# Kernel tuning notes

Measured on AMD Instinct MI355X. Metric: run time of the kernel, lower is better.

## Reference

```python
import jax, jax.numpy as jnp
import numpy as np

# ---- static config (matches init_kwargs) ----
B, H, W = 4, 256, 256
TIN, F, P = 10, 4, 8          # time steps in, forecast steps, patch size
CIN = TIN + 2                  # x concatenated with 2-channel grid
E = 768                        # LATENT_DIMS
NB, BS = 8, 96                 # num_blocks, block_size = E // NB
HP, WP = H // P, W // P
MID = 4 * E                    # channel-mixer hidden (MLP_RATIO=4)
DEPTH = 4
LAM = 0.01                     # softshrink sparsity_threshold


def _gelu(t):
    return jax.nn.gelu(t, approximate=False)  # torch default GELU (erf)


def _shrink(t):
    return jnp.sign(t) * jnp.maximum(jnp.abs(t) - LAM, 0.0)


def _spectral(x, w1, b1, w2, b2):
    """SpectralConvBlockDiag: rfft2 -> block-diag complex MLP (GELU) -> softshrink -> irfft2 + residual."""
    bias = x
    b_, h_, w_, c_ = x.shape
    wf = w_ // 2 + 1
    xf = jnp.fft.rfft2(x, axes=(1, 2), norm='ortho').reshape(b_, h_, wf, NB, BS)
    xr, xi = jnp.real(xf), jnp.imag(xf)
    mm = lambda t, w: jnp.einsum('bhfni,nio->bhfno', t, w)
    # complex linear 1 + GELU on real/imag separately
    o1r = _gelu(mm(xr, w1[0]) - mm(xi, w1[1]) + b1[0])
    o1i = _gelu(mm(xi, w1[0]) + mm(xr, w1[1]) + b1[1])
    # complex linear 2 + softshrink
    o2r = _shrink(mm(o1r, w2[0]) - mm(o1i, w2[1]) + b2[0])
    o2i = _shrink(mm(o1i, w2[0]) + mm(o1r, w2[1]) + b2[1])
    xf = (o2r + 1j * o2i).reshape(b_, h_, wf, c_)
    out = jnp.fft.irfft2(xf, s=(h_, w_), axes=(1, 2), norm='ortho')
    return out + bias


def setup_inputs() -> dict:
    key = jax.random.key(0)
    ks = jax.random.split(key, 20)
    s = 0.02
    f32 = jnp.float32
    return {
        'x': jax.random.normal(ks[0], (B, H, W, TIN), f32),
        'grid': jax.random.uniform(ks[1], (B, H, W, 2), f32),
        'conv_w': s * jax.random.normal(ks[2], (E, CIN, P, P), f32),
        'conv_b': s * jax.random.normal(ks[3], (E,), f32),
        'pos_emb': s * jax.random.normal(ks[4], (HP, WP, E), f32),
        'w1': s * jax.random.normal(ks[5], (DEPTH, 2, NB, BS, BS), f32),
        'b1': s * jax.random.normal(ks[6], (DEPTH, 2, NB, BS), f32),
        'w2': s * jax.random.normal(ks[7], (DEPTH, 2, NB, BS, BS), f32),
        'b2': s * jax.random.normal(ks[8], (DEPTH, 2, NB, BS), f32),
        'fc1_w': s * jax.random.normal(ks[9], (DEPTH, E, MID), f32),
        'fc1_b': s * jax.random.normal(ks[10], (DEPTH, MID), f32),
        'fc2_w': s * jax.random.normal(ks[11], (DEPTH, MID, E), f32),
        'fc2_b': s * jax.random.normal(ks[12], (DEPTH, E), f32),
        'head_w1': s * jax.random.normal(ks[13], (E, 2 * E), f32),
        'head_b1': s * jax.random.normal(ks[14], (2 * E,), f32),
        'head_w2': s * jax.random.normal(ks[15], (2 * E, P * P), f32),
        'head_b2': s * jax.random.normal(ks[16], (P * P,), f32),
    }


def reference(x, grid, conv_w, conv_b, pos_emb, w1, b1, w2, b2,
              fc1_w, fc1_b, fc2_w, fc2_b, head_w1, head_b1, head_w2, head_b2):
    # concat grid channels and patch-embed (conv stride==kernel == patch einsum)
    z = jnp.concatenate([x, grid], axis=-1)                  # (B,H,W,CIN)
    patches = z.reshape(B, HP, P, WP, P, CIN)
    t = jnp.einsum('bhpwqc,ecpq->bhwe', patches, conv_w) + conv_b + pos_emb  # (B,HP,WP,E)
    states = []
    for _ in range(F):
        for d in range(DEPTH):                               # AFNOBoundariesBlock (no residual, identity norms)
            t = _spectral(t, w1[d], b1[d], w2[d], b2[d])
            t = _gelu(t @ fc1_w[d] + fc1_b[d]) @ fc2_w[d] + fc2_b[d]
        states.append(t)
    ls = jnp.stack(states, axis=1)                           # (B,F,HP,WP,E)
    h = _gelu(ls @ head_w1 + head_b1) @ head_w2 + head_b2    # (B,F,HP,WP,P*P)
    h = h.reshape(B, F, HP, WP, P, P, 1)
    h = jnp.transpose(h, (0, 6, 2, 4, 3, 5, 1)).reshape(B, 1, H, W, F)
    return jnp.squeeze(h, axis=1)                            # (B,H,W,F)
```

## Files before the change

### kernel.cpp

```cpp
#include <hip/hip_runtime.h>
#include <hip/hip_bf16.h>
#include <math.h>


typedef __attribute__((ext_vector_type(8))) _Float16 half8;
typedef __attribute__((ext_vector_type(4))) _Float16 half4v;
typedef __attribute__((ext_vector_type(4))) float float4v;

__device__ __forceinline__ float gelu_f(float v) {
    return 0.5f * v * (1.0f + erff(v * 0.70710678118654752f));
}
__device__ __forceinline__ float shrink_f(float v) {
    return (v > 0.01f) ? (v - 0.01f) : ((v < -0.01f) ? (v + 0.01f) : 0.0f);
}

#define STEP32 0.19634954084936207f

__device__ __forceinline__ void async16(const void* g, void* l) {
    __builtin_amdgcn_global_load_lds(
        (const __attribute__((address_space(1))) unsigned int*)g,
        (__attribute__((address_space(3))) unsigned int*)l, 16, 0, 0);
}

__global__ __launch_bounds__(256) void gather_patch(const float* __restrict__ x,
        const float* __restrict__ grd, _Float16* __restrict__ A)
{
    int idx = blockIdx.x * 256 + threadIdx.x;
    int j   = idx % 768;
    int tok = idx / 768;
    int c = j >> 6, p = (j >> 3) & 7, q = j & 7;
    int wp = tok & 31, hp = (tok >> 5) & 31, b = tok >> 10;
    int hh = hp * 8 + p, ww = wp * 8 + q;
    float v;
    if (c < 10) v = x[((b * 256 + hh) * 256 + ww) * 10 + c];
    else        v = grd[((b * 256 + hh) * 256 + ww) * 2 + (c - 10)];
    A[idx] = (_Float16)v;
}

__global__ __launch_bounds__(256) void dft_fwd_w(const _Float16* __restrict__ th,
        _Float16* __restrict__ Xr, _Float16* __restrict__ Xi)
{
    __shared__ float2 lut[32];
    int bh = blockIdx.x;
    int tid = threadIdx.x;
    if (tid < 32) { float a = tid * STEP32; lut[tid] = make_float2(cosf(a), sinf(a)); }
    __syncthreads();
    int b = bh >> 5, h = bh & 31;
    int c = blockIdx.y * 256 + tid;
    float v[32];
    #pragma unroll
    for (int w = 0; w < 32; ++w) v[w] = (float)th[(bh * 32 + w) * 768 + c];
    for (int kw = 0; kw <= 16; ++kw) {
        float ar = 0.f, ai = 0.f;
        #pragma unroll
        for (int w = 0; w < 32; ++w) {
            float2 cs = lut[(kw * w) & 31];
            ar += v[w] * cs.x;
            ai -= v[w] * cs.y;
        }
        size_t g = ((size_t)(b * 17 + kw) * 32 + h) * 768 + c;
        Xr[g] = (_Float16)(ar * 0.03125f);
        Xi[g] = (_Float16)(ai * 0.03125f);
    }
}

__global__ __launch_bounds__(256) void idft_w_mfma(const _Float16* __restrict__ Yr,
        const _Float16* __restrict__ Yi, _Float16* __restrict__ th)
{
    __shared__ alignas(16) _Float16 Yt[192 * 40];
    __shared__ alignas(16) _Float16 El[32 * 40];

    const int tid  = threadIdx.x;
    const int wave = tid >> 6;
    const int lane = tid & 63;
    const int lr   = lane & 15;
    const int quad = lane >> 4;

    const int bh = blockIdx.x;
    const int b  = bh >> 5, h = bh & 31;
    const int c0 = blockIdx.y * 192;

    for (int i = tid; i < 1024; i += 256) {
        int w = i >> 5, s = i & 31;
        float val;
        if (s <= 16) {
            float g = (s == 0 || s == 16) ? 1.f : 2.f;
            val = g * cosf(((w * s) & 31) * STEP32) * 0.03125f;
        } else {
            int k = s - 16;
            val = -2.f * sinf(((w * k) & 31) * STEP32) * 0.03125f;
        }
        El[w * 40 + s] = (_Float16)val;
    }

    #pragma unroll
    for (int i = 0; i < 3; ++i) {
        int u    = tid + i * 256;
        int slot = u / 24;
        int cg   = u % 24;
        const _Float16* src;
        if (slot < 17) src = Yr + ((size_t)(b * 17 + slot) * 32 + h) * 768;
        else           src = Yi + ((size_t)(b * 17 + (slot - 16)) * 32 + h) * 768;
        half8 v = *(const half8*)(src + c0 + cg * 8);
        #pragma unroll
        for (int e = 0; e < 8; ++e) {
            int el = e ^ (cg & 7);
            Yt[(cg * 8 + el) * 40 + slot] = v[el];
        }
    }
    __syncthreads();

    half8 af[2], bf[3];
    #pragma unroll
    for (int m = 0; m < 2; ++m)
        af[m] = *(const half8*)&El[(m * 16 + lr) * 40 + quad * 8];
    #pragma unroll
    for (int n = 0; n < 3; ++n)
        bf[n] = *(const half8*)&Yt[(wave * 48 + n * 16 + lr) * 40 + quad * 8];
    float4v acc[2][3];
    #pragma unroll
    for (int m = 0; m < 2; ++m)
        #pragma unroll
        for (int n = 0; n < 3; ++n) {
            float4v z = {0.f, 0.f, 0.f, 0.f};
            acc[m][n] = __builtin_amdgcn_mfma_f32_16x16x32_f16(af[m], bf[n], z, 0, 0, 0);
        }

    #pragma unroll
    for (int m = 0; m < 2; ++m)
        #pragma unroll
        for (int n = 0; n < 3; ++n) {
            int c = c0 + wave * 48 + n * 16 + lr;
            #pragma unroll
            for (int r = 0; r < 4; ++r) {
                int w = m * 16 + quad * 4 + r;
                size_t gi = (size_t)(bh * 32 + w) * 768 + c;
                th[gi] = (_Float16)(acc[m][n][r] + (float)th[gi]);
            }
        }
}

__global__ __launch_bounds__(256) void prep_specw(const float* __restrict__ w1,
        const float* __restrict__ w2, _Float16* __restrict__ out)
{
    __shared__ float tile[96][97];
    int mid = blockIdx.x;
    int n  = mid & 7;
    int ri = (mid >> 3) & 1;
    int l  = (mid >> 4) & 1;
    int d  = mid >> 5;
    const float* src = (l ? w2 : w1) + ((size_t)(d * 2 + ri) * 8 + n) * 9216;
    for (int idx = threadIdx.x; idx < 9216; idx += 256)
        tile[idx / 96][idx % 96] = src[idx];
    __syncthreads();
    _Float16* dst = out + (size_t)mid * 9216;
    for (int idx = threadIdx.x; idx < 9216; idx += 256)
        dst[idx] = (_Float16)tile[idx % 96][idx / 96];
}

__global__ __launch_bounds__(256) void spec_fused(
        _Float16* __restrict__ Xr, _Float16* __restrict__ Xi,
        const _Float16* __restrict__ W1r, const _Float16* __restrict__ W1i,
        const _Float16* __restrict__ W2r, const _Float16* __restrict__ W2i,
        const float* __restrict__ b1r, const float* __restrict__ b1i,
        const float* __restrict__ b2r, const float* __restrict__ b2i)
{
    __shared__ alignas(16) _Float16 Ec[1024], Es[1024];
    __shared__ alignas(16) _Float16 XTr[3840], XTi[3840];
    __shared__ alignas(16) _Float16 Zr[3328], Zi[3328];
    __shared__ alignas(16) _Float16 Sr[3328], Si[3328];

    const int bk = blockIdx.x;
    const int n  = blockIdx.y;
    const int tid = threadIdx.x;
    const int wave = tid >> 6, lane = tid & 63;
    const int wr = wave >> 1, wc = wave & 1;
    const int lr = lane & 15, quad = lane >> 4;
    const size_t base = (size_t)bk * 24576 + n * 96;

    for (int i = tid; i < 1024; i += 256) {
        int kh = i >> 5, h = i & 31;
        float a = ((kh * h) & 31) * STEP32;
        Ec[i] = (_Float16)cosf(a);
        Es[i] = (_Float16)sinf(a);
    }
    for (int i = tid; i < 384; i += 256) {
        int h = i / 12, cc = (i % 12) * 8;
        half8 vr = *(const half8*)(Xr + base + (size_t)h * 768 + cc);
        half8 vi = *(const half8*)(Xi + base + (size_t)h * 768 + cc);
        #pragma unroll
        for (int e = 0; e < 8; ++e) {
            XTr[(cc + e) * 40 + h] = vr[e];
            XTi[(cc + e) * 40 + h] = vi[e];
        }
    }
    __syncthreads();

    const _Float16* w1r = W1r + (size_t)n * 9216;
    const _Float16* w1i = W1i + (size_t)n * 9216;
    const _Float16* w2r = W2r + (size_t)n * 9216;
    const _Float16* w2i = W2i + (size_t)n * 9216;

    half8 eC = *(const half8*)&Ec[(wr * 16 + lr) * 32 + quad * 8];
    half8 eS = *(const half8*)&Es[(wr * 16 + lr) * 32 + quad * 8];
    half8 eSn = -eS;

    {
        float4v zr[3], zi[3];
        #pragma unroll
        for (int j = 0; j < 3; ++j) { float4v z = {0,0,0,0}; zr[j] = z; zi[j] = z; }
        #pragma unroll
        for (int j = 0; j < 3; ++j) {
            int c = wc * 48 + j * 16 + lr;
            half8 xr = *(const half8*)&XTr[c * 40 + quad * 8];
            half8 xi = *(const half8*)&XTi[c * 40 + quad * 8];
            zr[j] = __builtin_amdgcn_mfma_f32_16x16x32_f16(eC,  xr, zr[j], 0, 0, 0);
            zr[j] = __builtin_amdgcn_mfma_f32_16x16x32_f16(eS,  xi, zr[j], 0, 0, 0);
            zi[j] = __builtin_amdgcn_mfma_f32_16x16x32_f16(eC,  xi, zi[j], 0, 0, 0);
            zi[j] = __builtin_amdgcn_mfma_f32_16x16x32_f16(eSn, xr, zi[j], 0, 0, 0);
        }
        #pragma unroll
        for (int j = 0; j < 3; ++j) {
            int c = wc * 48 + j * 16 + lr;
            #pragma unroll
            for (int r = 0; r < 4; ++r) {
                int kh = wr * 16 + quad * 4 + r;
                Zr[kh * 104 + c] = (_Float16)zr[j][r];
                Zi[kh * 104 + c] = (_Float16)zi[j][r];
            }
        }
    }
    __syncthreads();

    {
        float4v sr[3], si[3];
        #pragma unroll
        for (int j = 0; j < 3; ++j) { float4v z = {0,0,0,0}; sr[j] = z; si[j] = z; }
        #pragma unroll
        for (int kc = 0; kc < 3; ++kc) {
            half8 ar = *(const half8*)&Zr[(wr * 16 + lr) * 104 + kc * 32 + quad * 8];
            half8 ai = *(const half8*)&Zi[(wr * 16 + lr) * 104 + kc * 32 + quad * 8];
            half8 ain = -ai;
            #pragma unroll
            for (int j = 0; j < 3; ++j) {
                int o = wc * 48 + j * 16 + lr;
                half8 br = *(const half8*)&w1r[o * 96 + kc * 32 + quad * 8];
                half8 bi = *(const half8*)&w1i[o * 96 + kc * 32 + quad * 8];
                sr[j] = __builtin_amdgcn_mfma_f32_16x16x32_f16(ar,  br, sr[j], 0, 0, 0);
                sr[j] = __builtin_amdgcn_mfma_f32_16x16x32_f16(ain, bi, sr[j], 0, 0, 0);
                si[j] = __builtin_amdgcn_mfma_f32_16x16x32_f16(ai,  br, si[j], 0, 0, 0);
                si[j] = __builtin_amdgcn_mfma_f32_16x16x32_f16(ar,  bi, si[j], 0, 0, 0);
            }
        }
        #pragma unroll
        for (int j = 0; j < 3; ++j) {
            int o = wc * 48 + j * 16 + lr;
            float br = b1r[n * 96 + o], bi = b1i[n * 96 + o];
            #pragma unroll
            for (int r = 0; r < 4; ++r) {
                int kh = wr * 16 + quad * 4 + r;
                Sr[kh * 104 + o] = (_Float16)gelu_f(sr[j][r] + br);
                Si[kh * 104 + o] = (_Float16)gelu_f(si[j][r] + bi);
            }
        }
    }
    __syncthreads();

    {
        float4v tr[3], ti[3];
        #pragma unroll
        for (int j = 0; j < 3; ++j) { float4v z = {0,0,0,0}; tr[j] = z; ti[j] = z; }
        #pragma unroll
        for (int kc = 0; kc < 3; ++kc) {
            half8 ar = *(const half8*)&Sr[(wr * 16 + lr) * 104 + kc * 32 + quad * 8];
            half8 ai = *(const half8*)&Si[(wr * 16 + lr) * 104 + kc * 32 + quad * 8];
            half8 ain = -ai;
            #pragma unroll
            for (int j = 0; j < 3; ++j) {
                int o = wc * 48 + j * 16 + lr;
                half8 br = *(const half8*)&w2r[o * 96 + kc * 32 + quad * 8];
                half8 bi = *(const half8*)&w2i[o * 96 + kc * 32 + quad * 8];
                tr[j] = __builtin_amdgcn_mfma_f32_16x16x32_f16(ar,  br, tr[j], 0, 0, 0);
                tr[j] = __builtin_amdgcn_mfma_f32_16x16x32_f16(ain, bi, tr[j], 0, 0, 0);
                ti[j] = __builtin_amdgcn_mfma_f32_16x16x32_f16(ai,  br, ti[j], 0, 0, 0);
                ti[j] = __builtin_amdgcn_mfma_f32_16x16x32_f16(ar,  bi, ti[j], 0, 0, 0);
            }
        }
        #pragma unroll
        for (int j = 0; j < 3; ++j) {
            int o = wc * 48 + j * 16 + lr;
            float br = b2r[n * 96 + o], bi = b2i[n * 96 + o];
            #pragma unroll
            for (int r = 0; r < 4; ++r) {
                int kh = wr * 16 + quad * 4 + r;
                XTr[o * 40 + kh] = (_Float16)shrink_f(tr[j][r] + br);
                XTi[o * 40 + kh] = (_Float16)shrink_f(ti[j][r] + bi);
            }
        }
    }
    __syncthreads();

    {
        float4v yr[3], yi[3];
        #pragma unroll
        for (int j = 0; j < 3; ++j) { float4v z = {0,0,0,0}; yr[j] = z; yi[j] = z; }
        #pragma unroll
        for (int j = 0; j < 3; ++j) {
            int c = wc * 48 + j * 16 + lr;
            half8 t2r = *(const half8*)&XTr[c * 40 + quad * 8];
            half8 t2i = *(const half8*)&XTi[c * 40 + quad * 8];
            yr[j] = __builtin_amdgcn_mfma_f32_16x16x32_f16(eC,  t2r, yr[j], 0, 0, 0);
            yr[j] = __builtin_amdgcn_mfma_f32_16x16x32_f16(eSn, t2i, yr[j], 0, 0, 0);
            yi[j] = __builtin_amdgcn_mfma_f32_16x16x32_f16(eC,  t2i, yi[j], 0, 0, 0);
            yi[j] = __builtin_amdgcn_mfma_f32_16x16x32_f16(eS,  t2r, yi[j], 0, 0, 0);
        }
        #pragma unroll
        for (int j = 0; j < 3; ++j) {
            int c = wc * 48 + j * 16 + lr;
            #pragma unroll
            for (int r = 0; r < 4; ++r) {
                int h = wr * 16 + quad * 4 + r;
                Zr[h * 104 + c] = (_Float16)yr[j][r];
                Zi[h * 104 + c] = (_Float16)yi[j][r];
            }
        }
    }
    __syncthreads();

    for (int i = tid; i < 384; i += 256) {
        int h = i / 12, cc = (i % 12) * 8;
        half8 vr = *(const half8*)&Zr[h * 104 + cc];
        half8 vi = *(const half8*)&Zi[h * 104 + cc];
        *(half8*)(Xr + base + (size_t)h * 768 + cc) = vr;
        *(half8*)(Xi + base + (size_t)h * 768 + cc) = vi;
    }
}

__global__ __launch_bounds__(256) void cvt_f16(const float* __restrict__ in,
        _Float16* __restrict__ out)
{
    int i = blockIdx.x * 256 + threadIdx.x;
    float4 v = ((const float4*)in)[i];
    half4v o;
    o.x = (_Float16)v.x; o.y = (_Float16)v.y; o.z = (_Float16)v.z; o.w = (_Float16)v.w;
    ((half4v*)out)[i] = o;
}

__global__ __launch_bounds__(256) void cvt_transpose(const float* __restrict__ in,
        _Float16* __restrict__ out, int K, int N)
{
    __shared__ float tile[32][33];
    int kb = blockIdx.x * 32, nb = blockIdx.y * 32;
    int tx = threadIdx.x & 31, ty = threadIdx.x >> 5;
    #pragma unroll
    for (int r = 0; r < 32; r += 8)
        tile[ty + r][tx] = in[(size_t)(kb + ty + r) * N + nb + tx];
    __syncthreads();
    #pragma unroll
    for (int r = 0; r < 32; r += 8)
        out[(size_t)(nb + ty + r) * K + kb + tx] = (_Float16)tile[tx][ty + r];
}

template<int BN, int ACT>
__global__ __launch_bounds__(512, 4) void gemm128d(const _Float16* __restrict__ A,
        const _Float16* __restrict__ Bt, const float* __restrict__ bias,
        _Float16* __restrict__ C16, int M, int N, int K)
{
    constexpr int WN  = BN / 4;
    constexpr int FN  = WN / 16;
    constexpr int AU  = 2;
    constexpr int BU  = BN / 64;
    constexpr int LPT = AU + BU;
    __shared__ _Float16 Al[2][128 * 64];
    __shared__ _Float16 Bl[2][BN * 64];

    const int tid  = threadIdx.x;
    const int wave = tid >> 6;
    const int lane = tid & 63;
    const int wr   = wave >> 2;
    const int wc   = wave & 3;
    const int lr   = lane & 15;
    const int quad = lane >> 4;

    const int gx = gridDim.x, gy = gridDim.y, nbk = gx * gy;
    int bx = blockIdx.x, by = blockIdx.y;
    if (!(gy & 3) && !(gx & 1)) {
        int id = by * gx + bx;
        int xcd = id & 7, j = id >> 3;
        int cols = gx >> 1;
        int rows = gy >> 2;
        int jr = j / cols, jc = j % cols;
        by = (xcd >> 1) * rows + jr;
        bx = (xcd & 1) * cols + jc;
    } else if (!(nbk & 7)) {
        int id  = by * gx + bx;
        int id2 = (id & 7) * (nbk >> 3) + (id >> 3);
        by = id2 / gx; bx = id2 % gx;
    }
    const int row0 = by * 128;
    const int col0 = bx * BN;

    const int srow = lane >> 3;
    const int schk = (lane & 7) ^ (srow & 7);
    const _Float16* Ab = A  + (size_t)(row0 + wave * 8 + srow) * K + schk * 8;
    const _Float16* Bb = Bt + (size_t)(col0 + wave * 8 + srow) * K + schk * 8;

    auto stage = [&](int b, int kt) {
        const int k0 = kt * 64;
        #pragma unroll
        for (int u = 0; u < AU; ++u)
            async16(Ab + (size_t)u * 64 * K + k0, &Al[b][(u * 64 + wave * 8) * 64]);
        #pragma unroll
        for (int u = 0; u < BU; ++u)
            async16(Bb + (size_t)u * 64 * K + k0, &Bl[b][(u * 64 + wave * 8) * 64]);
    };

    float4v acc[4][FN];
    #pragma unroll
    for (int m = 0; m < 4; ++m)
        #pragma unroll
        for (int n = 0; n < FN; ++n) {
            float4v z = {0.f, 0.f, 0.f, 0.f};
            acc[m][n] = z;
        }

    auto compute = [&](int cb) {
        #pragma unroll
        for (int ks = 0; ks < 2; ++ks) {
            const int cA = ((ks * 4 + quad) ^ (lr & 7)) * 8;
            half8 bf[FN];
            #pragma unroll
            for (int n = 0; n < FN; ++n)
                bf[n] = *(const half8*)&Bl[cb][(wc * WN + n * 16 + lr) * 64 + cA];
            half8 af[4];
            #pragma unroll
            for (int m = 0; m < 4; ++m)
                af[m] = *(const half8*)&Al[cb][(wr * 64 + m * 16 + lr) * 64 + cA];
            __builtin_amdgcn_s_setprio(1);
            #pragma unroll
            for (int m = 0; m < 4; ++m)
                #pragma unroll
                for (int n = 0; n < FN; ++n)
                    acc[m][n] = __builtin_amdgcn_mfma_f32_16x16x32_f16(af[m], bf[n], acc[m][n], 0, 0, 0);
            __builtin_amdgcn_s_setprio(0);
        }
    };

    const int NT = K >> 6;
    stage(0, 0);
    stage(1, 1);
    for (int t = 0; t < NT; ++t) {
        if (t + 1 < NT) asm volatile("s_waitcnt vmcnt(5)" ::: "memory");
        else            asm volatile("s_waitcnt vmcnt(0)" ::: "memory");
        __builtin_amdgcn_s_barrier();
        compute(t & 1);
        __builtin_amdgcn_s_barrier();
        if (t + 2 < NT) stage(t & 1, t + 2);
    }

    #pragma unroll
    for (int n = 0; n < FN; ++n) {
        int col = col0 + wc * WN + n * 16 + lr;
        float bj = bias[col];
        #pragma unroll
        for (int m = 0; m < 4; ++m) {
            int row = row0 + wr * 64 + m * 16 + quad * 4;
            #pragma unroll
            for (int r = 0; r < 4; ++r) {
                float v = acc[m][n][r] + bj;
                if (ACT) v = gelu_f(v);
                C16[(size_t)(row + r) * N + col] = (_Float16)v;
            }
        }
    }
}

__global__ __launch_bounds__(256, 2) void fc2_fused(const _Float16* __restrict__ A,
        const _Float16* __restrict__ Bt, const float* __restrict__ bias,
        _Float16* __restrict__ C16, _Float16* __restrict__ XR,
        _Float16* __restrict__ XI)
{
    constexpr int K = 3072;
    constexpr int NT = 48;
    __shared__ _Float16 Al[2][64 * 64];
    __shared__ _Float16 Bl[2][96 * 64];
    __shared__ alignas(16) _Float16 Tl[2 * 96 * 40];
    __shared__ alignas(16) _Float16 ECl[1024], ESl[1024];

    const int tid  = threadIdx.x;
    const int wave = tid >> 6;
    const int lane = tid & 63;
    const int wr   = wave >> 1;
    const int wc   = wave & 1;
    const int lr   = lane & 15;
    const int quad = lane >> 4;

    for (int i = tid; i < 1024; i += 256) {
        int kw = i >> 5, w = i & 31;
        float a = ((kw * w) & 31) * STEP32;
        ECl[i] = (_Float16)(cosf(a) * 0.03125f);
        ESl[i] = (_Float16)(-sinf(a) * 0.03125f);
    }

    const int gx = gridDim.x, gy = gridDim.y;
    int bx = blockIdx.x, by = blockIdx.y;
    {
        int id = by * gx + bx;
        int xcd = id & 7, j = id >> 3;
        int cols = gx >> 1;
        int rows = gy >> 2;
        int jr = j / cols, jc = j % cols;
        by = (xcd >> 1) * rows + jr;
        bx = (xcd & 1) * cols + jc;
    }
    const int row0 = by * 64;
    const int col0 = bx * 96;

    const int srow = lane >> 3;
    const int schk = (lane & 7) ^ srow;
    const _Float16* Ab = A  + (size_t)(row0 + wave * 8 + srow) * K + schk * 8;
    const _Float16* Bb = Bt + (size_t)(col0 + wave * 8 + srow) * K + schk * 8;

    auto stage = [&](int b, int kt) {
        const int k0 = kt * 64;
        #pragma unroll
        for (int u = 0; u < 2; ++u)
            async16(Ab + (size_t)u * 32 * K + k0, &Al[b][(u * 32 + wave * 8) * 64]);
        #pragma unroll
        for (int u = 0; u < 3; ++u)
            async16(Bb + (size_t)u * 32 * K + k0, &Bl[b][(u * 32 + wave * 8) * 64]);
    };

    float4v acc[2][3];
    #pragma unroll
    for (int m = 0; m < 2; ++m)
        #pragma unroll
        for (int n = 0; n < 3; ++n) {
            float4v z = {0.f, 0.f, 0.f, 0.f};
            acc[m][n] = z;
        }

    auto compute = [&](int cb) {
        #pragma unroll
        for (int ks = 0; ks < 2; ++ks) {
            const int cA = ((ks * 4 + quad) ^ (lr & 7)) * 8;
            half8 bf[3];
            #pragma unroll
            for (int n = 0; n < 3; ++n)
                bf[n] = *(const half8*)&Bl[cb][(wc * 48 + n * 16 + lr) * 64 + cA];
            half8 af[2];
            #pragma unroll
            for (int m = 0; m < 2; ++m)
                af[m] = *(const half8*)&Al[cb][(wr * 32 + m * 16 + lr) * 64 + cA];
            __builtin_amdgcn_s_setprio(1);
            #pragma unroll
            for (int m = 0; m < 2; ++m)
                #pragma unroll
                for (int n = 0; n < 3; ++n)
                    acc[m][n] = __builtin_amdgcn_mfma_f32_16x16x32_f16(af[m], bf[n], acc[m][n], 0, 0, 0);
            __builtin_amdgcn_s_setprio(0);
        }
    };

    stage(0, 0);
    stage(1, 1);
    for (int t = 0; t < NT; ++t) {
        if (t + 1 < NT) asm volatile("s_waitcnt vmcnt(5)" ::: "memory");
        else            asm volatile("s_waitcnt vmcnt(0)" ::: "memory");
        __builtin_amdgcn_s_barrier();
        compute(t & 1);
        __builtin_amdgcn_s_barrier();
        if (t + 2 < NT) stage(t & 1, t + 2);
    }

    #pragma unroll
    for (int n = 0; n < 3; ++n) {
        int cc  = wc * 48 + n * 16 + lr;
        int col = col0 + cc;
        float bj = bias[col];
        #pragma unroll
        for (int m = 0; m < 2; ++m) {
            int row = row0 + wr * 32 + m * 16 + quad * 4;
            #pragma unroll
            for (int r = 0; r < 4; ++r) {
                float v = acc[m][n][r] + bj;
                C16[(size_t)(row + r) * 768 + col] = (_Float16)v;
                int lrow = row + r - row0;
                Tl[((lrow >> 5) * 96 + cc) * 40 + (lrow & 31)] = (_Float16)v;
            }
        }
    }
    __syncthreads();

    const int h     = wave >> 1;
    const int cbase = (wave & 1) * 48;
    const int b     = row0 >> 10;
    const int hp    = ((row0 >> 5) & 31) + h;
    half8 eC0 = *(const half8*)&ECl[lr * 32 + quad * 8];
    half8 eC1 = *(const half8*)&ECl[(16 + lr) * 32 + quad * 8];
    half8 eS0 = *(const half8*)&ESl[lr * 32 + quad * 8];
    half8 eS1 = *(const half8*)&ESl[(16 + lr) * 32 + quad * 8];
    float4v xr[2][3], xi[2][3];
    #pragma unroll
    for (int m = 0; m < 2; ++m)
        #pragma unroll
        for (int nj = 0; nj < 3; ++nj) {
            float4v z = {0.f, 0.f, 0.f, 0.f};
            xr[m][nj] = z; xi[m][nj] = z;
        }
    #pragma unroll
    for (int nj = 0; nj < 3; ++nj) {
        half8 tb = *(const half8*)&Tl[(h * 96 + cbase + nj * 16 + lr) * 40 + quad * 8];
        xr[0][nj] = __builtin_amdgcn_mfma_f32_16x16x32_f16(eC0, tb, xr[0][nj], 0, 0, 0);
        xr[1][nj] = __builtin_amdgcn_mfma_f32_16x16x32_f16(eC1, tb, xr[1][nj], 0, 0, 0);
        xi[0][nj] = __builtin_amdgcn_mfma_f32_16x16x32_f16(eS0, tb, xi[0][nj], 0, 0, 0);
        xi[1][nj] = __builtin_amdgcn_mfma_f32_16x16x32_f16(eS1, tb, xi[1][nj], 0, 0, 0);
    }
    #pragma unroll
    for (int m = 0; m < 2; ++m)
        #pragma unroll
        for (int r = 0; r < 4; ++r) {
            int kw = m * 16 + quad * 4 + r;
            if (kw < 17) {
                #pragma unroll
                for (int nj = 0; nj < 3; ++nj) {
                    int c = col0 + cbase + nj * 16 + lr;
                    size_t g = ((size_t)(b * 17 + kw) * 32 + hp) * 768 + c;
                    XR[g] = (_Float16)xr[m][nj][r];
                    XI[g] = (_Float16)xi[m][nj][r];
                }
            }
        }
}

__global__ __launch_bounds__(256, 4) void head2_k(const _Float16* __restrict__ A,
        const _Float16* __restrict__ Bt, const float* __restrict__ bias,
        float* __restrict__ C32, int f_idx)
{
    constexpr int K = 1536;
    constexpr int NT = 24;
    __shared__ _Float16 Al[2][64 * 64];
    __shared__ _Float16 Bl[2][64 * 64];

    const int tid  = threadIdx.x;
    const int wave = tid >> 6;
    const int lane = tid & 63;
    const int wr   = wave >> 1;
    const int wc   = wave & 1;
    const int lr   = lane & 15;
    const int quad = lane >> 4;

    const int row0 = blockIdx.x * 64;

    const int srow = lane >> 3;
    const int schk = (lane & 7) ^ srow;
    const _Float16* Ab = A  + (size_t)(row0 + wave * 8 + srow) * K + schk * 8;
    const _Float16* Bb = Bt + (size_t)(wave * 8 + srow) * K + schk * 8;

    auto stage = [&](int b, int kt) {
        const int k0 = kt * 64;
        #pragma unroll
        for (int u = 0; u < 2; ++u)
            async16(Ab + (size_t)u * 32 * K + k0, &Al[b][(u * 32 + wave * 8) * 64]);
        #pragma unroll
        for (int u = 0; u < 2; ++u)
            async16(Bb + (size_t)u * 32 * K + k0, &Bl[b][(u * 32 + wave * 8) * 64]);
    };

    float4v acc[2][2];
    #pragma unroll
    for (int m = 0; m < 2; ++m)
        #pragma unroll
        for (int n = 0; n < 2; ++n) {
            float4v z = {0.f, 0.f, 0.f, 0.f};
            acc[m][n] = z;
        }

    auto compute = [&](int cb) {
        #pragma unroll
        for (int ks = 0; ks < 2; ++ks) {
            const int cA = ((ks * 4 + quad) ^ (lr & 7)) * 8;
            half8 bf[2], af[2];
            #pragma unroll
            for (int n = 0; n < 2; ++n)
                bf[n] = *(const half8*)&Bl[cb][(wc * 32 + n * 16 + lr) * 64 + cA];
            #pragma unroll
            for (int m = 0; m < 2; ++m)
                af[m] = *(const half8*)&Al[cb][(wr * 32 + m * 16 + lr) * 64 + cA];
            #pragma unroll
            for (int m = 0; m < 2; ++m)
                #pragma unroll
                for (int n = 0; n < 2; ++n)
                    acc[m][n] = __builtin_amdgcn_mfma_f32_16x16x32_f16(af[m], bf[n], acc[m][n], 0, 0, 0);
        }
    };

    stage(0, 0);
    stage(1, 1);
    for (int t = 0; t < NT; ++t) {
        if (t + 1 < NT) asm volatile("s_waitcnt vmcnt(4)" ::: "memory");
        else            asm volatile("s_waitcnt vmcnt(0)" ::: "memory");
        __builtin_amdgcn_s_barrier();
        compute(t & 1);
        __builtin_amdgcn_s_barrier();
        if (t + 2 < NT) stage(t & 1, t + 2);
    }

    #pragma unroll
    for (int n = 0; n < 2; ++n) {
        int col = wc * 32 + n * 16 + lr;
        float bj = bias[col];
        int p = col >> 3, q = col & 7;
        #pragma unroll
        for (int m = 0; m < 2; ++m) {
            int row = row0 + wr * 32 + m * 16 + quad * 4;
            #pragma unroll
            for (int r = 0; r < 4; ++r) {
                float v = acc[m][n][r] + bj;
                int rowv = row + r;
                int bq = rowv >> 10, hp = (rowv >> 5) & 31, wp = rowv & 31;
                C32[(((size_t)(bq * 256 + hp * 8 + p)) * 256 + wp * 8 + q) * 4 + f_idx] = v;
            }
        }
    }
}

template<int BN, int OUT_MODE, int ACT>
__global__ __launch_bounds__(256) void gemm_h(const _Float16* __restrict__ A,
        const _Float16* __restrict__ Bt, const float* __restrict__ bias,
        const float* __restrict__ pos, float* __restrict__ C32,
        _Float16* __restrict__ C16, _Float16* __restrict__ XR,
        _Float16* __restrict__ XI, int M, int N, int K, int f_idx)
{
    constexpr int WN  = BN / 2;
    constexpr int FN  = WN / 16;
    constexpr int NBJ = BN / 64;
    constexpr int LPT = 2 + NBJ;
    __shared__ _Float16 Al[4][128 * 32];
    __shared__ _Float16 Bl[4][BN * 32];

    const int tid  = threadIdx.x;
    const int wave = tid >> 6;
    const int lane = tid & 63;
    const int wr   = wave >> 1;
    const int wc   = wave & 1;
    const int lr   = lane & 15;
    const int quad = lane >> 4;

    const int gx = gridDim.x, gy = gridDim.y, nbk = gx * gy;
    int bx = blockIdx.x, by = blockIdx.y;
    if (!(gy & 3) && !(gx & 1)) {
        int id = by * gx + bx;
        int xcd = id & 7, j = id >> 3;
        int cols = gx >> 1;
        int rows = gy >> 2;
        int jr = j / cols, jc = j % cols;
        by = (xcd >> 1) * rows + jr;
        bx = (xcd & 1) * cols + jc;
    } else if (!(nbk & 7)) {
        int id  = by * gx + bx;
        int id2 = (id & 7) * (nbk >> 3) + (id >> 3);
        by = id2 / gx; bx = id2 % gx;
    }
    const int row0 = by * 128;
    const int col0 = bx * BN;

    const int srow = lane >> 2;
    const int skof = ((lane & 3) ^ (srow & 3)) * 8;

    auto stage = [&](int b, int kt) {
        const int k0 = kt << 5;
        #pragma unroll
        for (int j = 0; j < 2; ++j)
            async16(A + (size_t)(row0 + j * 64 + wave * 16 + srow) * K + k0 + skof,
                    &Al[b][(j * 64 + wave * 16) * 32]);
        #pragma unroll
        for (int j = 0; j < NBJ; ++j)
            async16(Bt + (size_t)(col0 + j * 64 + wave * 16 + srow) * K + k0 + skof,
                    &Bl[b][(j * 64 + wave * 16) * 32]);
    };

    float4v acc[4][FN];
    #pragma unroll
    for (int i = 0; i < 4; ++i)
        #pragma unroll
        for (int j = 0; j < FN; ++j) {
            float4v z = {0.f, 0.f, 0.f, 0.f};
            acc[i][j] = z;
        }

    auto compute = [&](int cb) {
        const int cA = (quad ^ (lr & 3)) * 8;
        half8 af[4], bf[FN];
        #pragma unroll
        for (int i = 0; i < 4; ++i)
            af[i] = *(const half8*)&Al[cb][(wr * 64 + i * 16 + lr) * 32 + cA];
        #pragma unroll
        for (int j = 0; j < FN; ++j)
            bf[j] = *(const half8*)&Bl[cb][(wc * WN + j * 16 + lr) * 32 + cA];
        #pragma unroll
        for (int i = 0; i < 4; ++i)
            #pragma unroll
            for (int j = 0; j < FN; ++j)
                acc[i][j] = __builtin_amdgcn_mfma_f32_16x16x32_f16(af[i], bf[j], acc[i][j], 0, 0, 0);
    };

    const int KT = K >> 5;
    stage(0, 0); stage(1, 1); stage(2, 2);
    int kt = 0;
    for (; kt < KT - 3; ++kt) {
        stage((kt + 3) & 3, kt + 3);
        if constexpr (LPT == 4) asm volatile("s_waitcnt vmcnt(12)" ::: "memory");
        else                    asm volatile("s_waitcnt vmcnt(9)"  ::: "memory");
        __builtin_amdgcn_s_barrier();
        compute(kt & 3);
        asm volatile("" ::: "memory");
        __builtin_amdgcn_s_barrier();
    }
    if constexpr (LPT == 4) asm volatile("s_waitcnt vmcnt(8)" ::: "memory");
    else                    asm volatile("s_waitcnt vmcnt(6)" ::: "memory");
    __builtin_amdgcn_s_barrier();
    compute(kt & 3); ++kt;
    asm volatile("" ::: "memory");
    __builtin_amdgcn_s_barrier();
    if constexpr (LPT == 4) asm volatile("s_waitcnt vmcnt(4)" ::: "memory");
    else                    asm volatile("s_waitcnt vmcnt(3)" ::: "memory");
    __builtin_amdgcn_s_barrier();
    compute(kt & 3); ++kt;
    asm volatile("" ::: "memory");
    __builtin_amdgcn_s_barrier();
    asm volatile("s_waitcnt vmcnt(0)" ::: "memory");
    __builtin_amdgcn_s_barrier();
    compute(kt & 3);

    #pragma unroll
    for (int j = 0; j < FN; ++j) {
        int col = col0 + wc * WN + j * 16 + lr;
        float bj = bias[col];
        #pragma unroll
        for (int i = 0; i < 4; ++i) {
            int row = row0 + wr * 64 + i * 16 + quad * 4;
            #pragma unroll
            for (int r = 0; r < 4; ++r) {
                float v = acc[i][j][r] + bj;
                if (pos) v += pos[(size_t)((row + r) & 1023) * N + col];
                if (ACT) v = gelu_f(v);
                if (OUT_MODE == 3) {
                    int rowv = row + r;
                    int bq = rowv >> 10, hp = (rowv >> 5) & 31, wp = rowv & 31;
                    int p = col >> 3, q = col & 7;
                    C32[(((size_t)(bq * 256 + hp * 8 + p)) * 256 + wp * 8 + q) * 4 + f_idx] = v;
                } else {
                    C16[(size_t)(row + r) * N + col] = (_Float16)v;
                }
            }
        }
    }
}

extern "C" void kernel_launch(void* const* d_in, const int* in_sizes, int n_in,
                              void* d_out, int out_size, void* d_ws, size_t ws_size,
                              hipStream_t stream) {
    const float* x        = (const float*)d_in[0];
    const float* grd      = (const float*)d_in[1];
    const float* conv_w   = (const float*)d_in[2];
    const float* conv_b   = (const float*)d_in[3];
    const float* pos_emb  = (const float*)d_in[4];
    const float* w1       = (const float*)d_in[5];
    const float* b1       = (const float*)d_in[6];
    const float* w2       = (const float*)d_in[7];
    const float* b2       = (const float*)d_in[8];
    const float* fc1_w    = (const float*)d_in[9];
    const float* fc1_b    = (const float*)d_in[10];
    const float* fc2_w    = (const float*)d_in[11];
    const float* fc2_b    = (const float*)d_in[12];
    const float* head_w1  = (const float*)d_in[13];
    const float* head_b1  = (const float*)d_in[14];
    const float* head_w2  = (const float*)d_in[15];
    const float* head_b2  = (const float*)d_in[16];
    float* out = (float*)d_out;
    float* ws  = (float*)d_ws;

    float* pf = ws;
    _Float16* t_h     = (_Float16*)pf; pf += 1572864;
    _Float16* Wsp     = (_Float16*)pf; pf += 589824;
    _Float16* h1t     = (_Float16*)pf; pf += 589824;
    _Float16* h2t     = (_Float16*)pf; pf += 49152;
    _Float16* convw_h = (_Float16*)pf; pf += 294912;
    float* alias    = pf;              pf += 6291456;
    _Float16* hid_h = (_Float16*)alias;
    _Float16* WtAll = (_Float16*)pf;   pf += 9437184;
    _Float16* xa_r_fb = (_Float16*)alias;
    _Float16* xa_i_fb = (_Float16*)(alias + 835584);
    _Float16* xa_r_fu = (_Float16*)pf;
    _Float16* xa_i_fu = (_Float16*)(pf + 835584);
    size_t full_total = (size_t)(pf - ws) + 1671168;
    bool full = ws_size >= full_total * 4ull;
    _Float16* xa_r = full ? xa_r_fu : xa_r_fb;
    _Float16* xa_i = full ? xa_i_fu : xa_i_fb;
    _Float16* A_h  = (_Float16*)alias;

    prep_specw<<<dim3(128), 256, 0, stream>>>(w1, w2, Wsp);
    cvt_f16<<<dim3(576), 256, 0, stream>>>(conv_w, convw_h);
    cvt_transpose<<<dim3(24, 48), 256, 0, stream>>>(head_w1, h1t, 768, 1536);
    cvt_transpose<<<dim3(48, 2), 256, 0, stream>>>(head_w2, h2t, 1536, 64);
    for (int d = 0; d < 4; ++d) {
        cvt_transpose<<<dim3(24, 96), 256, 0, stream>>>(
            fc1_w + (size_t)d * 2359296, WtAll + (size_t)(2 * d) * 2359296, 768, 3072);
        cvt_transpose<<<dim3(96, 24), 256, 0, stream>>>(
            fc2_w + (size_t)d * 2359296, WtAll + (size_t)(2 * d + 1) * 2359296, 3072, 768);
    }
    gather_patch<<<dim3(12288), 256, 0, stream>>>(x, grd, A_h);
    gemm_h<128, 1, 0><<<dim3(6, 32), 256, 0, stream>>>(
        A_h, convw_h, conv_b, pos_emb, nullptr, t_h, nullptr, nullptr, 4096, 768, 768, 0);
    dft_fwd_w<<<dim3(128, 3), 256, 0, stream>>>(t_h, xa_r, xa_i);

    for (int f = 0; f < 4; ++f) {
        for (int d = 0; d < 4; ++d) {
            spec_fused<<<dim3(68, 8), 256, 0, stream>>>(
                xa_r, xa_i,
                Wsp + (size_t)(d * 4 + 0) * 73728, Wsp + (size_t)(d * 4 + 1) * 73728,
                Wsp + (size_t)(d * 4 + 2) * 73728, Wsp + (size_t)(d * 4 + 3) * 73728,
                b1 + d * 1536, b1 + d * 1536 + 768,
                b2 + d * 1536, b2 + d * 1536 + 768);
            idft_w_mfma<<<dim3(128, 4), 256, 0, stream>>>(xa_r, xa_i, t_h);
            gemm128d<192, 1><<<dim3(16, 32), 512, 0, stream>>>(
                t_h, WtAll + (size_t)(2 * d) * 2359296, fc1_b + d * 3072,
                hid_h, 4096, 3072, 768);
            if (full) {
                fc2_fused<<<dim3(8, 64), 256, 0, stream>>>(
                    hid_h, WtAll + (size_t)(2 * d + 1) * 2359296, fc2_b + d * 768,
                    t_h, xa_r, xa_i);
            } else {
                gemm_h<64, 1, 0><<<dim3(12, 32), 256, 0, stream>>>(
                    hid_h, WtAll + (size_t)(2 * d + 1) * 2359296, fc2_b + d * 768,
                    nullptr, nullptr, t_h, nullptr, nullptr, 4096, 768, 3072, 0);
                dft_fwd_w<<<dim3(128, 3), 256, 0, stream>>>(t_h, xa_r, xa_i);
            }
        }
        gemm128d<192, 1><<<dim3(8, 32), 512, 0, stream>>>(
            t_h, h1t, head_b1, hid_h, 4096, 1536, 768);
        head2_k<<<dim3(64), 256, 0, stream>>>(
            hid_h, h2t, head_b2, out, f);
    }
}
```

Baseline: 1.755 ms.

## Widen spectral block to 12 waves and shrink fc2 tile to 64 columns

spec_fused moves from 4 waves, each computing three 16-column output tiles, to 12 waves (768 threads), each computing one 16x16 tile. This spreads the serial MFMA chains across more waves and cuts per-wave register use. fc2_fused narrows its N tile from 96 to 64 columns, which shrinks the LDS buffers, raises the occupancy hint to 3, and grows the grid from 8x64 to 12x64 blocks so more blocks are in flight. The cost is more redundant A-tile loads and DFT constant setup per block, plus higher barrier overhead in the larger spectral block.

```diff
diff --git a/kernel.cpp b/kernel.cpp
--- a/kernel.cpp
+++ b/kernel.cpp
@@ -158,7 +158,7 @@
         dst[idx] = (_Float16)tile[idx % 96][idx / 96];
 }
 
-__global__ __launch_bounds__(256) void spec_fused(
+__global__ __launch_bounds__(768) void spec_fused(
         _Float16* __restrict__ Xr, _Float16* __restrict__ Xi,
         const _Float16* __restrict__ W1r, const _Float16* __restrict__ W1i,
         const _Float16* __restrict__ W2r, const _Float16* __restrict__ W2i,
@@ -174,17 +174,18 @@
     const int n  = blockIdx.y;
     const int tid = threadIdx.x;
     const int wave = tid >> 6, lane = tid & 63;
-    const int wr = wave >> 1, wc = wave & 1;
+    const int wr = wave / 6;
+    const int wo = wave % 6;
     const int lr = lane & 15, quad = lane >> 4;
     const size_t base = (size_t)bk * 24576 + n * 96;
 
-    for (int i = tid; i < 1024; i += 256) {
+    for (int i = tid; i < 1024; i += 768) {
         int kh = i >> 5, h = i & 31;
         float a = ((kh * h) & 31) * STEP32;
         Ec[i] = (_Float16)cosf(a);
         Es[i] = (_Float16)sinf(a);
     }
-    for (int i = tid; i < 384; i += 256) {
+    for (int i = tid; i < 384; i += 768) {
         int h = i / 12, cc = (i % 12) * 8;
         half8 vr = *(const half8*)(Xr + base + (size_t)h * 768 + cc);
         half8 vi = *(const half8*)(Xi + base + (size_t)h * 768 + cc);
@@ -206,128 +207,92 @@
     half8 eSn = -eS;
 
     {
-        float4v zr[3], zi[3];
-        #pragma unroll
-        for (int j = 0; j < 3; ++j) { float4v z = {0,0,0,0}; zr[j] = z; zi[j] = z; }
-        #pragma unroll
-        for (int j = 0; j < 3; ++j) {
-            int c = wc * 48 + j * 16 + lr;
-            half8 xr = *(const half8*)&XTr[c * 40 + quad * 8];
-            half8 xi = *(const half8*)&XTi[c * 40 + quad * 8];
-            zr[j] = __builtin_amdgcn_mfma_f32_16x16x32_f16(eC,  xr, zr[j], 0, 0, 0);
-            zr[j] = __builtin_amdgcn_mfma_f32_16x16x32_f16(eS,  xi, zr[j], 0, 0, 0);
-            zi[j] = __builtin_amdgcn_mfma_f32_16x16x32_f16(eC,  xi, zi[j], 0, 0, 0);
-            zi[j] = __builtin_amdgcn_mfma_f32_16x16x32_f16(eSn, xr, zi[j], 0, 0, 0);
-        }
-        #pragma unroll
-        for (int j = 0; j < 3; ++j) {
-            int c = wc * 48 + j * 16 + lr;
-            #pragma unroll
-            for (int r = 0; r < 4; ++r) {
-                int kh = wr * 16 + quad * 4 + r;
-                Zr[kh * 104 + c] = (_Float16)zr[j][r];
-                Zi[kh * 104 + c] = (_Float16)zi[j][r];
-            }
+        int c = wo * 16 + lr;
+        float4v zr = {0,0,0,0}, zi = {0,0,0,0};
+        half8 xr = *(const half8*)&XTr[c * 40 + quad * 8];
+        half8 xi = *(const half8*)&XTi[c * 40 + quad * 8];
+        zr = __builtin_amdgcn_mfma_f32_16x16x32_f16(eC,  xr, zr, 0, 0, 0);
+        zr = __builtin_amdgcn_mfma_f32_16x16x32_f16(eS,  xi, zr, 0, 0, 0);
+        zi = __builtin_amdgcn_mfma_f32_16x16x32_f16(eC,  xi, zi, 0, 0, 0);
+        zi = __builtin_amdgcn_mfma_f32_16x16x32_f16(eSn, xr, zi, 0, 0, 0);
+        #pragma unroll
+        for (int r = 0; r < 4; ++r) {
+            int kh = wr * 16 + quad * 4 + r;
+            Zr[kh * 104 + c] = (_Float16)zr[r];
+            Zi[kh * 104 + c] = (_Float16)zi[r];
         }
     }
     __syncthreads();
 
     {
-        float4v sr[3], si[3];
-        #pragma unroll
-        for (int j = 0; j < 3; ++j) { float4v z = {0,0,0,0}; sr[j] = z; si[j] = z; }
+        int o = wo * 16 + lr;
+        float4v sr = {0,0,0,0}, si = {0,0,0,0};
         #pragma unroll
         for (int kc = 0; kc < 3; ++kc) {
             half8 ar = *(const half8*)&Zr[(wr * 16 + lr) * 104 + kc * 32 + quad * 8];
             half8 ai = *(const half8*)&Zi[(wr * 16 + lr) * 104 + kc * 32 + quad * 8];
             half8 ain = -ai;
-            #pragma unroll
-            for (int j = 0; j < 3; ++j) {
-                int o = wc * 48 + j * 16 + lr;
-                half8 br = *(const half8*)&w1r[o * 96 + kc * 32 + quad * 8];
-                half8 bi = *(const half8*)&w1i[o * 96 + kc * 32 + quad * 8];
-                sr[j] = __builtin_amdgcn_mfma_f32_16x16x32_f16(ar,  br, sr[j], 0, 0, 0);
-                sr[j] = __builtin_amdgcn_mfma_f32_16x16x32_f16(ain, bi, sr[j], 0, 0, 0);
-                si[j] = __builtin_amdgcn_mfma_f32_16x16x32_f16(ai,  br, si[j], 0, 0, 0);
-                si[j] = __builtin_amdgcn_mfma_f32_16x16x32_f16(ar,  bi, si[j], 0, 0, 0);
-            }
-        }
-        #pragma unroll
-        for (int j = 0; j < 3; ++j) {
-            int o = wc * 48 + j * 16 + lr;
-            float br = b1r[n * 96 + o], bi = b1i[n * 96 + o];
-            #pragma unroll
-            for (int r = 0; r < 4; ++r) {
-                int kh = wr * 16 + quad * 4 + r;
-                Sr[kh * 104 + o] = (_Float16)gelu_f(sr[j][r] + br);
-                Si[kh * 104 + o] = (_Float16)gelu_f(si[j][r] + bi);
-            }
+            half8 br = *(const half8*)&w1r[o * 96 + kc * 32 + quad * 8];
+            half8 bi = *(const half8*)&w1i[o * 96 + kc * 32 + quad * 8];
+            sr = __builtin_amdgcn_mfma_f32_16x16x32_f16(ar,  br, sr, 0, 0, 0);
+            sr = __builtin_amdgcn_mfma_f32_16x16x32_f16(ain, bi, sr, 0, 0, 0);
+            si = __builtin_amdgcn_mfma_f32_16x16x32_f16(ai,  br, si, 0, 0, 0);
+            si = __builtin_amdgcn_mfma_f32_16x16x32_f16(ar,  bi, si, 0, 0, 0);
+        }
+        float br = b1r[n * 96 + o], bi = b1i[n * 96 + o];
+        #pragma unroll
+        for (int r = 0; r < 4; ++r) {
+            int kh = wr * 16 + quad * 4 + r;
+            Sr[kh * 104 + o] = (_Float16)gelu_f(sr[r] + br);
+            Si[kh * 104 + o] = (_Float16)gelu_f(si[r] + bi);
         }
     }
     __syncthreads();
 
     {
-        float4v tr[3], ti[3];
-        #pragma unroll
-        for (int j = 0; j < 3; ++j) { float4v z = {0,0,0,0}; tr[j] = z; ti[j] = z; }
+        int o = wo * 16 + lr;
+        float4v tr = {0,0,0,0}, ti = {0,0,0,0};
         #pragma unroll
         for (int kc = 0; kc < 3; ++kc) {
             half8 ar = *(const half8*)&Sr[(wr * 16 + lr) * 104 + kc * 32 + quad * 8];
             half8 ai = *(const half8*)&Si[(wr * 16 + lr) * 104 + kc * 32 + quad * 8];
             half8 ain = -ai;
-            #pragma unroll
-            for (int j = 0; j < 3; ++j) {
-                int o = wc * 48 + j * 16 + lr;
-                half8 br = *(const half8*)&w2r[o * 96 + kc * 32 + quad * 8];
-                half8 bi = *(const half8*)&w2i[o * 96 + kc * 32 + quad * 8];
-                tr[j] = __builtin_amdgcn_mfma_f32_16x16x32_f16(ar,  br, tr[j], 0, 0, 0);
-                tr[j] = __builtin_amdgcn_mfma_f32_16x16x32_f16(ain, bi, tr[j], 0, 0, 0);
-                ti[j] = __builtin_amdgcn_mfma_f32_16x16x32_f16(ai,  br, ti[j], 0, 0, 0);
-                ti[j] = __builtin_amdgcn_mfma_f32_16x16x32_f16(ar,  bi, ti[j], 0, 0, 0);
-            }
-        }
-        #pragma unroll
-        for (int j = 0; j < 3; ++j) {
-            int o = wc * 48 + j * 16 + lr;
-            float br = b2r[n * 96 + o], bi = b2i[n * 96 + o];
-            #pragma unroll
-            for (int r = 0; r < 4; ++r) {
-                int kh = wr * 16 + quad * 4 + r;
-                XTr[o * 40 + kh] = (_Float16)shrink_f(tr[j][r] + br);
-                XTi[o * 40 + kh] = (_Float16)shrink_f(ti[j][r] + bi);
-            }
+            half8 br = *(const half8*)&w2r[o * 96 + kc * 32 + quad * 8];
+            half8 bi = *(const half8*)&w2i[o * 96 + kc * 32 + quad * 8];
+            tr = __builtin_amdgcn_mfma_f32_16x16x32_f16(ar,  br, tr, 0, 0, 0);
+            tr = __builtin_amdgcn_mfma_f32_16x16x32_f16(ain, bi, tr, 0, 0, 0);
+            ti = __builtin_amdgcn_mfma_f32_16x16x32_f16(ai,  br, ti, 0, 0, 0);
+            ti = __builtin_amdgcn_mfma_f32_16x16x32_f16(ar,  bi, ti, 0, 0, 0);
+        }
+        float br = b2r[n * 96 + o], bi = b2i[n * 96 + o];
+        #pragma unroll
+        for (int r = 0; r < 4; ++r) {
+            int kh = wr * 16 + quad * 4 + r;
+            XTr[o * 40 + kh] = (_Float16)shrink_f(tr[r] + br);
+            XTi[o * 40 + kh] = (_Float16)shrink_f(ti[r] + bi);
         }
     }
     __syncthreads();
 
     {
-        float4v yr[3], yi[3];
-        #pragma unroll
-        for (int j = 0; j < 3; ++j) { float4v z = {0,0,0,0}; yr[j] = z; yi[j] = z; }
-        #pragma unroll
-        for (int j = 0; j < 3; ++j) {
-            int c = wc * 48 + j * 16 + lr;
-            half8 t2r = *(const half8*)&XTr[c * 40 + quad * 8];
-            half8 t2i = *(const half8*)&XTi[c * 40 + quad * 8];
-            yr[j] = __builtin_amdgcn_mfma_f32_16x16x32_f16(eC,  t2r, yr[j], 0, 0, 0);
-            yr[j] = __builtin_amdgcn_mfma_f32_16x16x32_f16(eSn, t2i, yr[j], 0, 0, 0);
-            yi[j] = __builtin_amdgcn_mfma_f32_16x16x32_f16(eC,  t2i, yi[j], 0, 0, 0);
-            yi[j] = __builtin_amdgcn_mfma_f32_16x16x32_f16(eS,  t2r, yi[j], 0, 0, 0);
-        }
-        #pragma unroll
-        for (int j = 0; j < 3; ++j) {
-            int c = wc * 48 + j * 16 + lr;
-            #pragma unroll
-            for (int r = 0; r < 4; ++r) {
-                int h = wr * 16 + quad * 4 + r;
-                Zr[h * 104 + c] = (_Float16)yr[j][r];
-                Zi[h * 104 + c] = (_Float16)yi[j][r];
-            }
+        int c = wo * 16 + lr;
+        float4v yr = {0,0,0,0}, yi = {0,0,0,0};
+        half8 t2r = *(const half8*)&XTr[c * 40 + quad * 8];
+        half8 t2i = *(const half8*)&XTi[c * 40 + quad * 8];
+        yr = __builtin_amdgcn_mfma_f32_16x16x32_f16(eC,  t2r, yr, 0, 0, 0);
+        yr = __builtin_amdgcn_mfma_f32_16x16x32_f16(eSn, t2i, yr, 0, 0, 0);
+        yi = __builtin_amdgcn_mfma_f32_16x16x32_f16(eC,  t2i, yi, 0, 0, 0);
+        yi = __builtin_amdgcn_mfma_f32_16x16x32_f16(eS,  t2r, yi, 0, 0, 0);
+        #pragma unroll
+        for (int r = 0; r < 4; ++r) {
+            int h = wr * 16 + quad * 4 + r;
+            Zr[h * 104 + c] = (_Float16)yr[r];
+            Zi[h * 104 + c] = (_Float16)yi[r];
         }
     }
     __syncthreads();
 
-    for (int i = tid; i < 384; i += 256) {
+    for (int i = tid; i < 384; i += 768) {
         int h = i / 12, cc = (i % 12) * 8;
         half8 vr = *(const half8*)&Zr[h * 104 + cc];
         half8 vi = *(const half8*)&Zi[h * 104 + cc];
@@ -475,7 +440,7 @@
     }
 }
 
-__global__ __launch_bounds__(256, 2) void fc2_fused(const _Float16* __restrict__ A,
+__global__ __launch_bounds__(256, 3) void fc2_fused(const _Float16* __restrict__ A,
         const _Float16* __restrict__ Bt, const float* __restrict__ bias,
         _Float16* __restrict__ C16, _Float16* __restrict__ XR,
         _Float16* __restrict__ XI)
@@ -483,8 +448,8 @@
     constexpr int K = 3072;
     constexpr int NT = 48;
     __shared__ _Float16 Al[2][64 * 64];
-    __shared__ _Float16 Bl[2][96 * 64];
-    __shared__ alignas(16) _Float16 Tl[2 * 96 * 40];
+    __shared__ _Float16 Bl[2][64 * 64];
+    __shared__ alignas(16) _Float16 Tl[2 * 64 * 40];
     __shared__ alignas(16) _Float16 ECl[1024], ESl[1024];
 
     const int tid  = threadIdx.x;
@@ -514,7 +479,7 @@
         bx = (xcd & 1) * cols + jc;
     }
     const int row0 = by * 64;
-    const int col0 = bx * 96;
+    const int col0 = bx * 64;
 
     const int srow = lane >> 3;
     const int schk = (lane & 7) ^ srow;
@@ -527,15 +492,15 @@
         for (int u = 0; u < 2; ++u)
             async16(Ab + (size_t)u * 32 * K + k0, &Al[b][(u * 32 + wave * 8) * 64]);
         #pragma unroll
-        for (int u = 0; u < 3; ++u)
+        for (int u = 0; u < 2; ++u)
             async16(Bb + (size_t)u * 32 * K + k0, &Bl[b][(u * 32 + wave * 8) * 64]);
     };
 
-    float4v acc[2][3];
+    float4v acc[2][2];
     #pragma unroll
     for (int m = 0; m < 2; ++m)
         #pragma unroll
-        for (int n = 0; n < 3; ++n) {
+        for (int n = 0; n < 2; ++n) {
             float4v z = {0.f, 0.f, 0.f, 0.f};
             acc[m][n] = z;
         }
@@ -544,11 +509,10 @@
         #pragma unroll
         for (int ks = 0; ks < 2; ++ks) {
             const int cA = ((ks * 4 + quad) ^ (lr & 7)) * 8;
-            half8 bf[3];
-            #pragma unroll
-            for (int n = 0; n < 3; ++n)
-                bf[n] = *(const half8*)&Bl[cb][(wc * 48 + n * 16 + lr) * 64 + cA];
-            half8 af[2];
+            half8 bf[2], af[2];
+            #pragma unroll
+            for (int n = 0; n < 2; ++n)
+                bf[n] = *(const half8*)&Bl[cb][(wc * 32 + n * 16 + lr) * 64 + cA];
             #pragma unroll
             for (int m = 0; m < 2; ++m)
                 af[m] = *(const half8*)&Al[cb][(wr * 32 + m * 16 + lr) * 64 + cA];
@@ -556,7 +520,7 @@
             #pragma unroll
             for (int m = 0; m < 2; ++m)
                 #pragma unroll
-                for (int n = 0; n < 3; ++n)
+                for (int n = 0; n < 2; ++n)
                     acc[m][n] = __builtin_amdgcn_mfma_f32_16x16x32_f16(af[m], bf[n], acc[m][n], 0, 0, 0);
             __builtin_amdgcn_s_setprio(0);
         }
@@ -565,7 +529,7 @@
     stage(0, 0);
     stage(1, 1);
     for (int t = 0; t < NT; ++t) {
-        if (t + 1 < NT) asm volatile("s_waitcnt vmcnt(5)" ::: "memory");
+        if (t + 1 < NT) asm volatile("s_waitcnt vmcnt(4)" ::: "memory");
         else            asm volatile("s_waitcnt vmcnt(0)" ::: "memory");
         __builtin_amdgcn_s_barrier();
         compute(t & 1);
@@ -574,8 +538,8 @@
     }
 
     #pragma unroll
-    for (int n = 0; n < 3; ++n) {
-        int cc  = wc * 48 + n * 16 + lr;
+    for (int n = 0; n < 2; ++n) {
+        int cc  = wc * 32 + n * 16 + lr;
         int col = col0 + cc;
         float bj = bias[col];
         #pragma unroll
@@ -586,31 +550,31 @@
                 float v = acc[m][n][r] + bj;
                 C16[(size_t)(row + r) * 768 + col] = (_Float16)v;
                 int lrow = row + r - row0;
-                Tl[((lrow >> 5) * 96 + cc) * 40 + (lrow & 31)] = (_Float16)v;
+                Tl[((lrow >> 5) * 64 + cc) * 40 + (lrow & 31)] = (_Float16)v;
             }
         }
     }
     __syncthreads();
 
     const int h     = wave >> 1;
-    const int cbase = (wave & 1) * 48;
+    const int cbase = (wave & 1) * 32;
     const int b     = row0 >> 10;
     const int hp    = ((row0 >> 5) & 31) + h;
     half8 eC0 = *(const half8*)&ECl[lr * 32 + quad * 8];
     half8 eC1 = *(const half8*)&ECl[(16 + lr) * 32 + quad * 8];
     half8 eS0 = *(const half8*)&ESl[lr * 32 + quad * 8];
     half8 eS1 = *(const half8*)&ESl[(16 + lr) * 32 + quad * 8];
-    float4v xr[2][3], xi[2][3];
+    float4v xr[2][2], xi[2][2];
     #pragma unroll
     for (int m = 0; m < 2; ++m)
         #pragma unroll
-        for (int nj = 0; nj < 3; ++nj) {
+        for (int nj = 0; nj < 2; ++nj) {
             float4v z = {0.f, 0.f, 0.f, 0.f};
             xr[m][nj] = z; xi[m][nj] = z;
         }
     #pragma unroll
-    for (int nj = 0; nj < 3; ++nj) {
-        half8 tb = *(const half8*)&Tl[(h * 96 + cbase + nj * 16 + lr) * 40 + quad * 8];
+    for (int nj = 0; nj < 2; ++nj) {
+        half8 tb = *(const half8*)&Tl[(h * 64 + cbase + nj * 16 + lr) * 40 + quad * 8];
         xr[0][nj] = __builtin_amdgcn_mfma_f32_16x16x32_f16(eC0, tb, xr[0][nj], 0, 0, 0);
         xr[1][nj] = __builtin_amdgcn_mfma_f32_16x16x32_f16(eC1, tb, xr[1][nj], 0, 0, 0);
         xi[0][nj] = __builtin_amdgcn_mfma_f32_16x16x32_f16(eS0, tb, xi[0][nj], 0, 0, 0);
@@ -623,7 +587,7 @@
             int kw = m * 16 + quad * 4 + r;
             if (kw < 17) {
                 #pragma unroll
-                for (int nj = 0; nj < 3; ++nj) {
+                for (int nj = 0; nj < 2; ++nj) {
                     int c = col0 + cbase + nj * 16 + lr;
                     size_t g = ((size_t)(b * 17 + kw) * 32 + hp) * 768 + c;
                     XR[g] = (_Float16)xr[m][nj][r];
@@ -917,7 +881,7 @@
 
     for (int f = 0; f < 4; ++f) {
         for (int d = 0; d < 4; ++d) {
-            spec_fused<<<dim3(68, 8), 256, 0, stream>>>(
+            spec_fused<<<dim3(68, 8), 768, 0, stream>>>(
                 xa_r, xa_i,
                 Wsp + (size_t)(d * 4 + 0) * 73728, Wsp + (size_t)(d * 4 + 1) * 73728,
                 Wsp + (size_t)(d * 4 + 2) * 73728, Wsp + (size_t)(d * 4 + 3) * 73728,
@@ -928,7 +892,7 @@
                 t_h, WtAll + (size_t)(2 * d) * 2359296, fc1_b + d * 3072,
                 hid_h, 4096, 3072, 768);
             if (full) {
-                fc2_fused<<<dim3(8, 64), 256, 0, stream>>>(
+                fc2_fused<<<dim3(12, 64), 256, 0, stream>>>(
                     hid_h, WtAll + (size_t)(2 * d + 1) * 2359296, fc2_b + d * 768,
                     t_h, xa_r, xa_i);
             } else {
```

Result: faster. 1.701 ms (-3.1%).
